# Performance work log

Measured on AMD Instinct MI355X. Metric: run time of the kernel, lower is better.

Reference implementation:

```python
import jax, jax.numpy as jnp
import numpy as np

HIDDEN = 2048
HEADS = 16
HEAD_DIM = HIDDEN // HEADS
LATENT = 512
B, T = 2, 2048


def setup_inputs() -> dict:
    key = jax.random.key(0)
    ks = jax.random.split(key, 12)
    s = lambda fan_in: 1.0 / np.sqrt(fan_in)
    x = jax.random.normal(ks[0], (B, T, HIDDEN), dtype=jnp.float32)
    Wq = jax.random.uniform(ks[1], (HIDDEN, HIDDEN), jnp.float32, -s(HIDDEN), s(HIDDEN))
    bq = jax.random.uniform(ks[2], (HIDDEN,), jnp.float32, -s(HIDDEN), s(HIDDEN))
    Wl = jax.random.uniform(ks[3], (HIDDEN, LATENT), jnp.float32, -s(HIDDEN), s(HIDDEN))
    bl = jax.random.uniform(ks[4], (LATENT,), jnp.float32, -s(HIDDEN), s(HIDDEN))
    # per-head back-projections stacked along head axis: [H, latent, head_dim]
    Wk = jax.random.uniform(ks[5], (HEADS, LATENT, HEAD_DIM), jnp.float32, -s(LATENT), s(LATENT))
    bk = jax.random.uniform(ks[6], (HEADS, HEAD_DIM), jnp.float32, -s(LATENT), s(LATENT))
    Wv = jax.random.uniform(ks[7], (HEADS, LATENT, HEAD_DIM), jnp.float32, -s(LATENT), s(LATENT))
    bv = jax.random.uniform(ks[8], (HEADS, HEAD_DIM), jnp.float32, -s(LATENT), s(LATENT))
    Wo = jax.random.uniform(ks[9], (HIDDEN, HIDDEN), jnp.float32, -s(HIDDEN), s(HIDDEN))
    bo = jax.random.uniform(ks[10], (HIDDEN,), jnp.float32, -s(HIDDEN), s(HIDDEN))
    return {"x": x, "Wq": Wq, "bq": bq, "Wl": Wl, "bl": bl,
            "Wk": Wk, "bk": bk, "Wv": Wv, "bv": bv, "Wo": Wo, "bo": bo}


def reference(x, Wq, bq, Wl, bl, Wk, bk, Wv, bv, Wo, bo):
    Bc, Tc, _ = x.shape
    # Q projection, split into heads: [B, H, T, Dh]
    q = (x @ Wq + bq).reshape(Bc, Tc, HEADS, HEAD_DIM).transpose(0, 2, 1, 3)
    # shared low-rank latent KV (cache=None -> just new tokens): [B, T, L]
    latent = x @ Wl + bl
    # per-head back-projections fused as one grouped matmul: [B, H, T, Dh]
    k = jnp.einsum('btl,hld->bhtd', latent, Wk) + bk[None, :, None, :]
    v = jnp.einsum('btl,hld->bhtd', latent, Wv) + bv[None, :, None, :]
    # full (non-causal) attention, matching the original module
    scores = jnp.einsum('bhqd,bhkd->bhqk', q, k) / np.sqrt(HEAD_DIM).astype(jnp.float32)
    probs = jax.nn.softmax(scores, axis=-1)
    attn = jnp.einsum('bhqk,bhkd->bhqd', probs, v)
    attn = attn.transpose(0, 2, 1, 3).reshape(Bc, Tc, HIDDEN)
    return attn @ Wo + bo
```

## Files before the change

kernel.cpp:

```cpp
#include <hip/hip_runtime.h>
#include <hip/hip_bf16.h>
#include <cstdint>

#define SEQ     2048
#define NHID    2048
#define NLAT    512
#define NHEAD   16
#define DHEAD   128
#define NBATCH  2
#define NROWS   (NBATCH*SEQ)

typedef unsigned short u16;
typedef __attribute__((ext_vector_type(8))) short short8;
typedef __attribute__((ext_vector_type(4))) float f32x4;

#define MFMA16 __builtin_amdgcn_mfma_f32_16x16x32_bf16

__device__ __forceinline__ u16 f2b(float f) {
    uint32_t u = __float_as_uint(f);
    uint32_t r = (u + 0x7fffu + ((u >> 16) & 1u)) >> 16;
    return (u16)r;
}

__device__ __forceinline__ void async16(const u16* g, u16* l) {
    __builtin_amdgcn_global_load_lds(
        (const __attribute__((address_space(1))) unsigned int*)g,
        (__attribute__((address_space(3))) unsigned int*)l, 16, 0, 0);
}

__device__ __forceinline__ void stage_lds(const u16* __restrict__ src, size_t strideE,
                                          u16* lds, int wave, int lane,
                                          int log2cpr, int xmask, int reps, int nlanes) {
    const int cmask = (1 << log2cpr) - 1;
    for (int rep = 0; rep < reps; ++rep) {
        int cbase = rep * nlanes + wave * 64;
        int ci = cbase + lane;
        int row = ci >> log2cpr;
        int sc = ci & cmask;
        int dchunk = sc ^ (row & xmask);
        const u16* g = src + (size_t)row * strideE + dchunk * 8;
        async16(g, lds + (size_t)cbase * 8);
    }
}

__global__ __launch_bounds__(256) void prep(const float* __restrict__ x,
                                            const float* __restrict__ Wq,
                                            const float* __restrict__ Wl,
                                            const float* __restrict__ Wk,
                                            const float* __restrict__ Wv,
                                            const float* __restrict__ Wo,
                                            u16* __restrict__ xb,
                                            u16* __restrict__ WqlT,
                                            u16* __restrict__ WkvT,
                                            u16* __restrict__ WoT) {
    const int t = blockIdx.x, tid = threadIdx.x;
    if (t < 8192) {
        int i = t * 256 + tid;
        float4 v = ((const float4*)x)[i];
        unsigned int lo = (unsigned int)f2b(v.x) | ((unsigned int)f2b(v.y) << 16);
        unsigned int hi = (unsigned int)f2b(v.z) | ((unsigned int)f2b(v.w) << 16);
        ((uint2*)xb)[i] = make_uint2(lo, hi);
        return;
    }
    __shared__ float tile[32][33];
    const float* src; u16* dst; int R, C, tY, tX;
    if (t < 12288)      { int tt = t - 8192;  src = Wq; dst = WqlT;           R = 2048; C = 2048; tY = tt >> 6; tX = tt & 63; }
    else if (t < 13312) { int tt = t - 12288; src = Wl; dst = WqlT + 4194304; R = 2048; C = 512;  tY = tt >> 4; tX = tt & 15; }
    else if (t < 14336) { int tt = t - 13312; int hh = tt >> 6; tt &= 63;
                          src = Wk + hh * 65536; dst = WkvT + hh * 65536;     R = 512;  C = 128;  tY = tt >> 2; tX = tt & 3; }
    else if (t < 15360) { int tt = t - 14336; int hh = tt >> 6; tt &= 63;
                          src = Wv + hh * 65536; dst = WkvT + 1048576 + hh * 65536;
                                                                              R = 512;  C = 128;  tY = tt >> 2; tX = tt & 3; }
    else                { int tt = t - 15360; src = Wo; dst = WoT;            R = 2048; C = 2048; tY = tt >> 6; tX = tt & 63; }
    const int tx = tid & 31, ty = tid >> 5;
    const int r0 = tY * 32, c0 = tX * 32;
    #pragma unroll
    for (int i = 0; i < 32; i += 8)
        tile[ty + i][tx] = src[(size_t)(r0 + ty + i) * C + c0 + tx];
    __syncthreads();
    #pragma unroll
    for (int i = 0; i < 32; i += 8)
        dst[(size_t)(c0 + ty + i) * R + r0 + tx] = f2b(tile[tx][ty + i]);
}

template<int STORE>
__global__ __launch_bounds__(256) void gemm_bt(const u16* __restrict__ A,
                                               const u16* __restrict__ Bt,
                                               const float* __restrict__ bias1,
                                               const float* __restrict__ bias2,
                                               void* __restrict__ C1,
                                               void* __restrict__ C2,
                                               int M, int N, int K) {
    __shared__ __align__(16) u16 As[128 * 32];
    __shared__ __align__(16) u16 Bs[128 * 32];
    const int tid = threadIdx.x, wave = tid >> 6, lane = tid & 63;
    const int quad = lane >> 4, m16 = lane & 15;
    const int m0 = blockIdx.y * 128, n0 = blockIdx.x * 128;
    const int wr = wave >> 1, wc = wave & 1;
    f32x4 acc[4][4] = {};
    for (int k0 = 0; k0 < K; k0 += 32) {
        __syncthreads();
        stage_lds(A + (size_t)m0 * K + k0, K, As, wave, lane, 2, 0, 2, 256);
        stage_lds(Bt + (size_t)n0 * K + k0, K, Bs, wave, lane, 2, 0, 2, 256);
        __syncthreads();
        short8 af[4], bfr[4];
        #pragma unroll
        for (int i = 0; i < 4; i++)
            af[i] = *(const short8*)&As[(wr * 64 + i * 16 + m16) * 32 + quad * 8];
        #pragma unroll
        for (int j = 0; j < 4; j++)
            bfr[j] = *(const short8*)&Bs[(wc * 64 + j * 16 + m16) * 32 + quad * 8];
        #pragma unroll
        for (int i = 0; i < 4; i++)
            #pragma unroll
            for (int j = 0; j < 4; j++)
                acc[i][j] = MFMA16(af[i], bfr[j], acc[i][j], 0, 0, 0);
    }
    const bool second = (n0 >= 2048);
    #pragma unroll
    for (int j = 0; j < 4; j++) {
        int n = n0 + wc * 64 + j * 16 + m16;
        float bv;
        if constexpr (STORE == 2) bv = bias1[n];
        else bv = second ? bias2[n - 2048] : bias1[n];
        #pragma unroll
        for (int i = 0; i < 4; i++) {
            int mrow = m0 + wr * 64 + i * 16 + quad * 4;
            if constexpr (STORE == 4) {
                if (second) {
                    int n2 = n - 2048;
                    ushort4 pk;
                    pk.x = f2b(acc[i][j][0] + bv);
                    pk.y = f2b(acc[i][j][1] + bv);
                    pk.z = f2b(acc[i][j][2] + bv);
                    pk.w = f2b(acc[i][j][3] + bv);
                    *(ushort4*)&((u16*)C2)[((size_t)((m0 >> 11) * 2048 + n2)) * 2048 +
                                           (mrow & 2047)] = pk;
                    continue;
                }
            }
            #pragma unroll
            for (int r = 0; r < 4; r++) {
                float v = acc[i][j][r] + bv;
                int m = mrow + r;
                if constexpr (STORE == 2)
                    ((float*)C1)[(size_t)m * N + n] = v;
                else if constexpr (STORE == 3) {
                    if (!second) ((u16*)C1)[(size_t)m * 2048 + n] = f2b(v);
                    else         ((u16*)C2)[(size_t)m * 512 + (n - 2048)] = f2b(v);
                } else {
                    ((u16*)C1)[(size_t)m * 2048 + n] = f2b(v);
                }
            }
        }
    }
}

__global__ __launch_bounds__(256, 2) void attn_fused(const u16* __restrict__ Q,
                                                     const u16* __restrict__ Kf,
                                                     const u16* __restrict__ Vt,
                                                     u16* __restrict__ Ob) {
    __shared__ __align__(16) u16 Kt[2][64 * 128];
    __shared__ __align__(16) u16 Vtile[2][128 * 64];
    __shared__ __align__(16) u16 Ps[4][32 * 64];
    const int tid = threadIdx.x, wave = tid >> 6, lane = tid & 63;
    const int quad = lane >> 4, m16 = lane & 15;
    const int bh = blockIdx.y, b = bh >> 4, h = bh & 15;
    const int q0 = blockIdx.x * 128;
    const size_t grow = (size_t)b * SEQ;
    const u16* Kbase = Kf + grow * NHID + h * DHEAD;
    const u16* Vbase = Vt + (grow + h * DHEAD) * SEQ;

    const u16* qsrc = Q + (grow + q0) * NHID + h * DHEAD;
    stage_lds(qsrc, NHID, Kt[0], wave, lane, 4, 15, 4, 256);
    stage_lds(qsrc + (size_t)64 * NHID, NHID, Kt[1], wave, lane, 4, 15, 4, 256);
    __syncthreads();
    short8 qf[2][4];
    {
        const u16* qbuf = Kt[wave >> 1];
        int rbase = (wave & 1) * 32;
        #pragma unroll
        for (int i = 0; i < 2; i++)
            #pragma unroll
            for (int c = 0; c < 4; c++)
                qf[i][c] = *(const short8*)&qbuf[(rbase + i * 16 + m16) * 128 +
                                                (((c * 4 + quad) ^ m16)) * 8];
    }
    __syncthreads();

    stage_lds(Kbase, NHID, Kt[0], wave, lane, 4, 15, 4, 256);
    stage_lds(Vbase, SEQ, Vtile[0], wave, lane, 3, 7, 4, 256);

    f32x4 o[2][8] = {};
    float lsum[2][4] = {};
    const float sc = 0.08838834764831845f;

    for (int it = 0; it < SEQ / 64; ++it) {
        const int cur = it & 1;
        __syncthreads();
        if (it + 1 < SEQ / 64) {
            stage_lds(Kbase + (size_t)(it + 1) * 64 * NHID, NHID, Kt[cur ^ 1],
                      wave, lane, 4, 15, 4, 256);
            stage_lds(Vbase + (it + 1) * 64, SEQ, Vtile[cur ^ 1],
                      wave, lane, 3, 7, 4, 256);
        }
        const u16* kt = Kt[cur];
        const u16* vt = Vtile[cur];

        f32x4 s[2][4] = {};
        #pragma unroll
        for (int c = 0; c < 4; c++)
            #pragma unroll
            for (int j = 0; j < 4; j++) {
                short8 kb = *(const short8*)&kt[(j * 16 + m16) * 128 +
                                               (((c * 4 + quad) ^ m16)) * 8];
                s[0][j] = MFMA16(qf[0][c], kb, s[0][j], 0, 0, 0);
                s[1][j] = MFMA16(qf[1][c], kb, s[1][j], 0, 0, 0);
            }

        u16* pw = Ps[wave];
        #pragma unroll
        for (int i = 0; i < 2; i++)
            #pragma unroll
            for (int r = 0; r < 4; r++) {
                int rowl = i * 16 + quad * 4 + r;
                #pragma unroll
                for (int j = 0; j < 4; j++) {
                    float p = __expf(s[i][j][r] * sc);
                    lsum[i][r] += p;
                    int slot = (2 * j + (m16 >> 3)) ^ (rowl & 7);
                    pw[rowl * 64 + slot * 8 + (m16 & 7)] = f2b(p);
                }
            }

        #pragma unroll
        for (int c2 = 0; c2 < 2; c2++) {
            short8 pa[2];
            #pragma unroll
            for (int i = 0; i < 2; i++)
                pa[i] = *(const short8*)&pw[(i * 16 + m16) * 64 +
                                            (((c2 * 4 + quad) ^ (m16 & 7))) * 8];
            #pragma unroll
            for (int jd = 0; jd < 8; jd++) {
                short8 vb = *(const short8*)&vt[(jd * 16 + m16) * 64 +
                                               (((c2 * 4 + quad) ^ (m16 & 7))) * 8];
                o[0][jd] = MFMA16(pa[0], vb, o[0][jd], 0, 0, 0);
                o[1][jd] = MFMA16(pa[1], vb, o[1][jd], 0, 0, 0);
            }
        }
    }

    #pragma unroll
    for (int i = 0; i < 2; i++) {
        float inv[4];
        #pragma unroll
        for (int r = 0; r < 4; r++) {
            float v = lsum[i][r];
            #pragma unroll
            for (int off = 1; off < 16; off <<= 1)
                v += __shfl_xor(v, off);
            inv[r] = 1.f / v;
        }
        #pragma unroll
        for (int jd = 0; jd < 8; jd++)
            #pragma unroll
            for (int r = 0; r < 4; r++) {
                int t = q0 + wave * 32 + i * 16 + quad * 4 + r;
                int d = jd * 16 + m16;
                Ob[(grow + t) * NHID + h * DHEAD + d] = f2b(o[i][jd][r] * inv[r]);
            }
    }
}

extern "C" void kernel_launch(void* const* d_in, const int* in_sizes, int n_in,
                              void* d_out, int out_size, void* d_ws, size_t ws_size,
                              hipStream_t stream) {
    const float* x  = (const float*)d_in[0];
    const float* Wq = (const float*)d_in[1];
    const float* bq = (const float*)d_in[2];
    const float* Wl = (const float*)d_in[3];
    const float* bl = (const float*)d_in[4];
    const float* Wk = (const float*)d_in[5];
    const float* bk = (const float*)d_in[6];
    const float* Wv = (const float*)d_in[7];
    const float* bv = (const float*)d_in[8];
    const float* Wo = (const float*)d_in[9];
    const float* bo = (const float*)d_in[10];
    float* out = (float*)d_out;

    u16* w = (u16*)d_ws;
    u16* xb    = w;
    u16* WqlT  = xb    + 8388608;
    u16* WkvT  = WqlT  + 5242880;
    u16* WoT   = WkvT  + 2097152;
    u16* qb    = WoT   + 4194304;
    u16* kb    = qb    + 8388608;
    u16* vt    = kb    + 8388608;
    u16* lat   = vt    + 8388608;
    u16* attnb = xb;

    prep<<<19456, 256, 0, stream>>>(x, Wq, Wl, Wk, Wv, Wo, xb, WqlT, WkvT, WoT);

    gemm_bt<3><<<dim3(20, 32), 256, 0, stream>>>(xb, WqlT, bq, bl, qb, lat,
                                                 NROWS, 2560, 2048);
    gemm_bt<4><<<dim3(32, 32), 256, 0, stream>>>(lat, WkvT, bk, bv, kb, vt,
                                                 NROWS, 4096, 512);

    attn_fused<<<dim3(16, 32), 256, 0, stream>>>(qb, kb, vt, attnb);

    gemm_bt<2><<<dim3(16, 32), 256, 0, stream>>>(attnb, WoT, bo, nullptr, out, nullptr,
                                                 NROWS, 2048, 2048);
}
```

Baseline: 403.2 us.

## Double-buffer GEMM LDS tiles and XOR-swizzle them to avoid bank conflicts

```diff
diff --git a/kernel.cpp b/kernel.cpp
--- a/kernel.cpp
+++ b/kernel.cpp
@@ -30,14 +30,15 @@
 
 __device__ __forceinline__ void stage_lds(const u16* __restrict__ src, size_t strideE,
                                           u16* lds, int wave, int lane,
-                                          int log2cpr, int xmask, int reps, int nlanes) {
+                                          int log2cpr, int xmask, int xshift,
+                                          int reps, int nlanes) {
     const int cmask = (1 << log2cpr) - 1;
     for (int rep = 0; rep < reps; ++rep) {
         int cbase = rep * nlanes + wave * 64;
         int ci = cbase + lane;
         int row = ci >> log2cpr;
         int sc = ci & cmask;
-        int dchunk = sc ^ (row & xmask);
+        int dchunk = sc ^ ((row >> xshift) & xmask);
         const u16* g = src + (size_t)row * strideE + dchunk * 8;
         async16(g, lds + (size_t)cbase * 8);
     }
@@ -91,25 +92,35 @@
                                                void* __restrict__ C1,
                                                void* __restrict__ C2,
                                                int M, int N, int K) {
-    __shared__ __align__(16) u16 As[128 * 32];
-    __shared__ __align__(16) u16 Bs[128 * 32];
+    __shared__ __align__(16) u16 As[2][128 * 32];
+    __shared__ __align__(16) u16 Bs[2][128 * 32];
     const int tid = threadIdx.x, wave = tid >> 6, lane = tid & 63;
     const int quad = lane >> 4, m16 = lane & 15;
     const int m0 = blockIdx.y * 128, n0 = blockIdx.x * 128;
     const int wr = wave >> 1, wc = wave & 1;
+    const int swz = (quad ^ ((m16 >> 1) & 3)) * 8;
+    const u16* Ab = A + (size_t)m0 * K;
+    const u16* Bb = Bt + (size_t)n0 * K;
+    const int KI = K >> 5;
+
+    stage_lds(Ab, K, As[0], wave, lane, 2, 3, 1, 2, 256);
+    stage_lds(Bb, K, Bs[0], wave, lane, 2, 3, 1, 2, 256);
+
     f32x4 acc[4][4] = {};
-    for (int k0 = 0; k0 < K; k0 += 32) {
+    for (int it = 0; it < KI; ++it) {
+        const int cur = it & 1;
         __syncthreads();
-        stage_lds(A + (size_t)m0 * K + k0, K, As, wave, lane, 2, 0, 2, 256);
-        stage_lds(Bt + (size_t)n0 * K + k0, K, Bs, wave, lane, 2, 0, 2, 256);
-        __syncthreads();
+        if (it + 1 < KI) {
+            stage_lds(Ab + (it + 1) * 32, K, As[cur ^ 1], wave, lane, 2, 3, 1, 2, 256);
+            stage_lds(Bb + (it + 1) * 32, K, Bs[cur ^ 1], wave, lane, 2, 3, 1, 2, 256);
+        }
         short8 af[4], bfr[4];
         #pragma unroll
         for (int i = 0; i < 4; i++)
-            af[i] = *(const short8*)&As[(wr * 64 + i * 16 + m16) * 32 + quad * 8];
+            af[i] = *(const short8*)&As[cur][(wr * 64 + i * 16 + m16) * 32 + swz];
         #pragma unroll
         for (int j = 0; j < 4; j++)
-            bfr[j] = *(const short8*)&Bs[(wc * 64 + j * 16 + m16) * 32 + quad * 8];
+            bfr[j] = *(const short8*)&Bs[cur][(wc * 64 + j * 16 + m16) * 32 + swz];
         #pragma unroll
         for (int i = 0; i < 4; i++)
             #pragma unroll
@@ -172,8 +183,8 @@
     const u16* Vbase = Vt + (grow + h * DHEAD) * SEQ;
 
     const u16* qsrc = Q + (grow + q0) * NHID + h * DHEAD;
-    stage_lds(qsrc, NHID, Kt[0], wave, lane, 4, 15, 4, 256);
-    stage_lds(qsrc + (size_t)64 * NHID, NHID, Kt[1], wave, lane, 4, 15, 4, 256);
+    stage_lds(qsrc, NHID, Kt[0], wave, lane, 4, 15, 0, 4, 256);
+    stage_lds(qsrc + (size_t)64 * NHID, NHID, Kt[1], wave, lane, 4, 15, 0, 4, 256);
     __syncthreads();
     short8 qf[2][4];
     {
@@ -188,8 +199,8 @@
     }
     __syncthreads();
 
-    stage_lds(Kbase, NHID, Kt[0], wave, lane, 4, 15, 4, 256);
-    stage_lds(Vbase, SEQ, Vtile[0], wave, lane, 3, 7, 4, 256);
+    stage_lds(Kbase, NHID, Kt[0], wave, lane, 4, 15, 0, 4, 256);
+    stage_lds(Vbase, SEQ, Vtile[0], wave, lane, 3, 7, 0, 4, 256);
 
     f32x4 o[2][8] = {};
     float lsum[2][4] = {};
@@ -200,9 +211,9 @@
         __syncthreads();
         if (it + 1 < SEQ / 64) {
             stage_lds(Kbase + (size_t)(it + 1) * 64 * NHID, NHID, Kt[cur ^ 1],
-                      wave, lane, 4, 15, 4, 256);
+                      wave, lane, 4, 15, 0, 4, 256);
             stage_lds(Vbase + (it + 1) * 64, SEQ, Vtile[cur ^ 1],
-                      wave, lane, 3, 7, 4, 256);
+                      wave, lane, 3, 7, 0, 4, 256);
         }
         const u16* kt = Kt[cur];
         const u16* vt = Vtile[cur];
```

New measurement: 356.9 us. 11.5% less time.
